# Optimization experiments

Measured on AMD Instinct MI355X. Metric: run time of the kernel, lower is better.

The kernel has to match this reference:

```python
import jax, jax.numpy as jnp
import numpy as np

D_MODEL = 1024
NUM_HEADS = 16
HEAD_DIM = D_MODEL // NUM_HEADS
NUM_KERNELS = 21


def tisa_bias(amp, off, sharp, seq_len):
    # amp/off/sharp: (H, K). Returns (H, L, L) translation-invariant bias.
    # Evaluate on the 2L-1 distinct relative distances, then gather (Toeplitz).
    d = jnp.arange(-(seq_len - 1), seq_len, dtype=amp.dtype)  # (2L-1,)
    # (H, K, 2L-1) -> sum over kernels -> (H, 2L-1)
    scores = jnp.sum(
        amp[:, :, None]
        * jnp.exp(-jnp.abs(sharp)[:, :, None] * (d[None, None, :] - off[:, :, None]) ** 2),
        axis=1,
    )
    i = jnp.arange(seq_len)
    rel_idx = i[None, :] - i[:, None] + (seq_len - 1)  # (L, L) in [0, 2L-2]
    return scores[:, rel_idx]  # (H, L, L)


def setup_inputs() -> dict:
    key = jax.random.key(0)
    ks = jax.random.split(key, 9)
    B, L = 4, 1024
    s = 0.02
    return {
        "x_q": jax.random.normal(ks[0], (B, L, D_MODEL), dtype=jnp.float32),
        "x_kv": jax.random.normal(ks[1], (B, L, D_MODEL), dtype=jnp.float32),
        "Wq": jax.random.normal(ks[2], (D_MODEL, D_MODEL), dtype=jnp.float32) * s,
        "Wm": jax.random.normal(ks[3], (D_MODEL, 2 * D_MODEL), dtype=jnp.float32) * s,
        "Wg": jax.random.normal(ks[4], (D_MODEL, 2 * D_MODEL), dtype=jnp.float32) * s,
        "bg": jnp.zeros((2 * D_MODEL,), dtype=jnp.float32),
        "tisa_amp": jax.random.normal(ks[5], (NUM_HEADS, NUM_KERNELS), dtype=jnp.float32) * 0.1,
        "tisa_off": jax.random.uniform(ks[6], (NUM_HEADS, NUM_KERNELS), dtype=jnp.float32, minval=-512.0, maxval=512.0),
        "tisa_sharp": jax.random.uniform(ks[7], (NUM_HEADS, NUM_KERNELS), dtype=jnp.float32, minval=1e-4, maxval=0.05),
    }


def reference(x_q, x_kv, Wq, Wm, Wg, bg, tisa_amp, tisa_off, tisa_sharp):
    B, Lq, _ = x_q.shape
    Lkv = x_kv.shape[1]
    H, Dh = NUM_HEADS, HEAD_DIM

    q = (x_q @ Wq).reshape(B, Lq, H, Dh).transpose(0, 2, 1, 3)        # (B,H,Lq,Dh)
    mem = (x_kv @ Wm)                                                 # (B,Lkv,2D)
    k = mem[..., :D_MODEL].reshape(B, Lkv, H, Dh).transpose(0, 2, 1, 3)
    v = mem[..., D_MODEL:].reshape(B, Lkv, H, Dh).transpose(0, 2, 1, 3)

    scale = 1.0 / jnp.sqrt(jnp.asarray(Dh, dtype=q.dtype))
    scores = jnp.einsum("bhqd,bhkd->bhqk", q, k) * scale              # (B,H,Lq,Lkv)
    scores = scores + tisa_bias(tisa_amp, tisa_off, tisa_sharp, Lkv)[None]
    weights = jax.nn.softmax(scores, axis=-1)

    attn = jnp.einsum("bhqk,bhkd->bhqd", weights, v)                  # (B,H,Lq,Dh)
    attn = attn.transpose(0, 2, 1, 3).reshape(B, Lq, D_MODEL)

    g = attn @ Wg + bg                                                # (B,Lq,2D)
    a, b = g[..., :D_MODEL], g[..., D_MODEL:]
    return a * jax.nn.sigmoid(b)
```

## Files before the change

### kernel.cpp

```cpp
#include <hip/hip_runtime.h>
#include <cstdint>
#include <cstddef>

typedef __attribute__((ext_vector_type(8))) short bf16x8;
typedef __attribute__((ext_vector_type(4))) float f32x4;

#define LOG2E 1.44269504f

__device__ __forceinline__ unsigned short f2bf(float x) {
  unsigned int u = __float_as_uint(x);
  u += 0x7FFFu + ((u >> 16) & 1u);
  return (unsigned short)(u >> 16);
}
__device__ __forceinline__ unsigned short f2bf_trunc(float x) {
  return (unsigned short)(__float_as_uint(x) >> 16);
}

__device__ __forceinline__ void gload_lds16(const void* g, void* l) {
  __builtin_amdgcn_global_load_lds(
      (const __attribute__((address_space(1))) unsigned int*)g,
      (__attribute__((address_space(3))) unsigned int*)l, 16, 0, 0);
}


__global__ void preproc(const float* __restrict__ x_q, const float* __restrict__ x_kv,
                        const float* __restrict__ Wq, const float* __restrict__ Wm,
                        const float* __restrict__ Wg,
                        const float* __restrict__ amp, const float* __restrict__ off,
                        const float* __restrict__ sharp,
                        ushort4* __restrict__ bXq, ushort4* __restrict__ bXkv,
                        unsigned short* __restrict__ dWq, unsigned short* __restrict__ dWm,
                        unsigned short* __restrict__ dWg, float* __restrict__ tab) {
  __shared__ float tile[32][33];
  const int blk = blockIdx.x;
  if (blk < 8192) {
    int i = blk * 256 + threadIdx.x;
    float4 v;
    ushort4* d;
    if (i < (1 << 20)) { v = ((const float4*)x_q)[i]; d = bXq + i; }
    else { int j = i - (1 << 20); v = ((const float4*)x_kv)[j]; d = bXkv + j; }
    ushort4 o;
    o.x = f2bf(v.x); o.y = f2bf(v.y); o.z = f2bf(v.z); o.w = f2bf(v.w);
    *d = o;
  } else if (blk < 14336) {
    int idx = blk - 8192;
    int z = idx >> 11, rem = idx & 2047;
    int bx = rem & 63, by = rem >> 6;
    const float* src = z == 0 ? Wq : (z == 1 ? Wm : Wg);
    unsigned short* dst = z == 0 ? dWq : (z == 1 ? dWm : dWg);
    int N = z == 0 ? 1024 : 2048;
    int nb = bx * 32, kb = by * 32;
    if (nb >= N) return;
    int tx = threadIdx.x & 31, ty = threadIdx.x >> 5;
#pragma unroll
    for (int r = ty; r < 32; r += 8)
      tile[r][tx] = src[(size_t)(kb + r) * N + nb + tx];
    __syncthreads();
#pragma unroll
    for (int r = ty; r < 32; r += 8)
      dst[(size_t)(nb + r) * 1024 + kb + tx] = f2bf(tile[tx][r]);
  } else {
    int h = blk - 14336;
    for (int idx = threadIdx.x; idx < 2047; idx += 256) {
      float d = (float)(idx - 1023);
      float acc = 0.f;
#pragma unroll
      for (int k = 0; k < 21; ++k) {
        float dd = d - off[h * 21 + k];
        acc += amp[h * 21 + k] * __expf(-fabsf(sharp[h * 21 + k]) * dd * dd);
      }
      tab[h * 2047 + idx] = acc * LOG2E;
    }
  }
}


__global__ __launch_bounds__(256, 4)
void qkv_gemm(const unsigned short* __restrict__ Xq,
              const unsigned short* __restrict__ Xkv,
              const unsigned short* __restrict__ WqT,
              const unsigned short* __restrict__ WmT,
              unsigned short* __restrict__ qbuf,
              unsigned short* __restrict__ kbuf,
              unsigned short* __restrict__ vtbuf) {
  __shared__ unsigned short sA[2][128 * 32];
  __shared__ unsigned short sB[2][128 * 32];
  const int bx = blockIdx.x;
  const bool isQ = bx < 8;
  const int ntile = (isQ ? bx : bx - 8) << 7;
  const unsigned short* A = isQ ? Xq : Xkv;
  const unsigned short* B = (isQ ? WqT : WmT) + (size_t)ntile * 1024;
  const int t = threadIdx.x, lane = t & 63, w = t >> 6;
  const int wm = (w >> 1) << 6, wn = (w & 1) << 6;
  const int mtile = blockIdx.y << 7;
  const int c = lane & 15, g = lane >> 4;
  const int srow = t >> 2, scol = (t & 3) << 3;
  const unsigned short* aP = A + (size_t)(mtile + srow) * 1024 + scol;
  const unsigned short* bP = B + (size_t)srow * 1024 + scol;
  const int lo = srow * 32 + scol;

  gload_lds16(aP, &sA[0][lo]);
  gload_lds16(aP + 64 * 1024, &sA[0][lo + 64 * 32]);
  gload_lds16(bP, &sB[0][lo]);
  gload_lds16(bP + 64 * 1024, &sB[0][lo + 64 * 32]);
  __syncthreads();

  f32x4 acc[4][4] = {};
  for (int kt = 0; kt < 32; ++kt) {
    const int cur = kt & 1;
    if (kt + 1 < 32) {
      const int ko = (kt + 1) * 32;
      gload_lds16(aP + ko, &sA[1 - cur][lo]);
      gload_lds16(aP + 64 * 1024 + ko, &sA[1 - cur][lo + 64 * 32]);
      gload_lds16(bP + ko, &sB[1 - cur][lo]);
      gload_lds16(bP + 64 * 1024 + ko, &sB[1 - cur][lo + 64 * 32]);
    }
    bf16x8 af[4], bfr[4];
#pragma unroll
    for (int i = 0; i < 4; ++i) {
      af[i]  = *(const bf16x8*)&sA[cur][(wm + i * 16 + c) * 32 + g * 8];
      bfr[i] = *(const bf16x8*)&sB[cur][(wn + i * 16 + c) * 32 + g * 8];
    }
#pragma unroll
    for (int i = 0; i < 4; ++i)
#pragma unroll
      for (int j = 0; j < 4; ++j)
        acc[i][j] = __builtin_amdgcn_mfma_f32_16x16x32_bf16(af[i], bfr[j], acc[i][j], 0, 0, 0);
    __syncthreads();
  }

  const int row0 = mtile + wm + (g << 2);
  const int col0 = ntile + wn + c;
  if (isQ) {
#pragma unroll
    for (int i = 0; i < 4; ++i)
#pragma unroll
      for (int j = 0; j < 4; ++j) {
        int r = row0 + i * 16, cl = col0 + j * 16;
#pragma unroll
        for (int ri = 0; ri < 4; ++ri)
          qbuf[(size_t)(r + ri) * 1024 + cl] = f2bf(acc[i][j][ri] * (0.125f * LOG2E));
      }
  } else {
#pragma unroll
    for (int i = 0; i < 4; ++i)
#pragma unroll
      for (int j = 0; j < 4; ++j) {
        int r = row0 + i * 16, cl = col0 + j * 16;
        if (cl < 1024) {
#pragma unroll
          for (int ri = 0; ri < 4; ++ri)
            kbuf[(size_t)(r + ri) * 1024 + cl] = f2bf(acc[i][j][ri]);
        } else {
          int d = cl - 1024;
          int hh = d >> 6, dh = d & 63;
          int bb = r >> 10, ll = r & 1023;
          ushort4 pk;
          pk.x = f2bf(acc[i][j][0]);
          pk.y = f2bf(acc[i][j][1]);
          pk.z = f2bf(acc[i][j][2]);
          pk.w = f2bf(acc[i][j][3]);
          *(ushort4*)&vtbuf[((size_t)((bb * 16 + hh) * 64 + dh) << 10) + ll] = pk;
        }
      }
  }
}


__global__ __launch_bounds__(512)
void attn_kernel(const unsigned short* __restrict__ qbuf,
                 const unsigned short* __restrict__ kbuf,
                 const unsigned short* __restrict__ vtbuf,
                 const float* __restrict__ biasTab,
                 unsigned short* __restrict__ attnb) {
  const int h = blockIdx.x & 15, b = blockIdx.x >> 4, qt = blockIdx.y;
  __shared__ unsigned short sK[2][64 * 64];
  __shared__ unsigned short sV[3][64 * 64];
  __shared__ unsigned short sP[2][128 * 64];
  __shared__ float sLsum[2][128];
  const int t = threadIdx.x, lane = t & 63, w = t >> 6;
  const int c = lane & 15, g = lane >> 4;
  const int rg = w >> 1, cg = w & 1;

  const int r = t >> 3, ch = (t & 7) ^ (r & 7);

  const unsigned short* qsrc = qbuf + (size_t)(b * 1024 + qt * 128) * 1024 + h * 64;
  const unsigned short* ksrc = kbuf + (size_t)(b * 1024) * 1024 + h * 64;
  const unsigned short* vsrc = vtbuf + (size_t)((b * 16 + h) * 64) * 1024;

  unsigned short* sQ = &sP[0][0];
  gload_lds16(qsrc + (size_t)r * 1024 + ch * 8, &sQ[t * 8]);
  gload_lds16(qsrc + (size_t)(r + 64) * 1024 + ch * 8, &sQ[4096 + t * 8]);
  gload_lds16(ksrc + (size_t)r * 1024 + ch * 8, &sK[0][t * 8]);
  gload_lds16(vsrc + (size_t)r * 1024 + ch * 8, &sV[0][t * 8]);
  __syncthreads();

  bf16x8 aq[2][2];
#pragma unroll
  for (int rf = 0; rf < 2; ++rf) {
    int row = rg * 32 + rf * 16 + c;
#pragma unroll
    for (int ks = 0; ks < 2; ++ks)
      aq[rf][ks] = *(const bf16x8*)&sQ[row * 64 + (((ks * 4 + g) ^ (row & 7)) * 8)];
  }
  __syncthreads();

  f32x4 o[2][2] = {};
  float lsum[2][4] = {};
  const float* bb = biasTab + h * 2047 + 1023 + cg * 32 + c - qt * 128 - rg * 32 - g * 4;

  int vcur = 0, vnx = 1;
  for (int kv = 0; kv < 16; ++kv) {
    const int cur = kv & 1;

    const float* bk = bb + kv * 64;
    f32x4 s[2][2];
#pragma unroll
    for (int rf = 0; rf < 2; ++rf)
#pragma unroll
      for (int nf = 0; nf < 2; ++nf)
#pragma unroll
        for (int ri = 0; ri < 4; ++ri)
          s[rf][nf][ri] = bk[(nf - rf) * 16 - ri];

    if (kv + 1 < 16) {
      gload_lds16(ksrc + (size_t)((kv + 1) * 64 + r) * 1024 + ch * 8, &sK[1 - cur][t * 8]);
      gload_lds16(vsrc + (size_t)r * 1024 + (kv + 1) * 64 + ch * 8, &sV[vnx][t * 8]);
    }

#pragma unroll
    for (int nf = 0; nf < 2; ++nf) {
      int krow = cg * 32 + nf * 16 + c;
      bf16x8 k0 = *(const bf16x8*)&sK[cur][krow * 64 + (((g) ^ (krow & 7)) * 8)];
      bf16x8 k1 = *(const bf16x8*)&sK[cur][krow * 64 + (((4 + g) ^ (krow & 7)) * 8)];
#pragma unroll
      for (int rf = 0; rf < 2; ++rf) {
        s[rf][nf] = __builtin_amdgcn_mfma_f32_16x16x32_bf16(aq[rf][0], k0, s[rf][nf], 0, 0, 0);
        s[rf][nf] = __builtin_amdgcn_mfma_f32_16x16x32_bf16(aq[rf][1], k1, s[rf][nf], 0, 0, 0);
      }
    }

#pragma unroll
    for (int rf = 0; rf < 2; ++rf)
#pragma unroll
      for (int nf = 0; nf < 2; ++nf)
#pragma unroll
        for (int ri = 0; ri < 4; ++ri) {
          float e = exp2f(s[rf][nf][ri]);
          lsum[rf][ri] += e;
          int prow = rg * 32 + rf * 16 + g * 4 + ri;
          int chunk = cg * 4 + nf * 2 + (c >> 3);
          sP[cur][prow * 64 + ((chunk ^ (prow & 7)) * 8) + (c & 7)] = f2bf_trunc(e);
        }
    __syncthreads();

    bf16x8 ap[2][2];
#pragma unroll
    for (int rf = 0; rf < 2; ++rf) {
      int row = rg * 32 + rf * 16 + c;
#pragma unroll
      for (int ks = 0; ks < 2; ++ks)
        ap[rf][ks] = *(const bf16x8*)&sP[cur][row * 64 + (((ks * 4 + g) ^ (row & 7)) * 8)];
    }
#pragma unroll
    for (int df = 0; df < 2; ++df) {
      int vrow = cg * 32 + df * 16 + c;
      bf16x8 v0 = *(const bf16x8*)&sV[vcur][vrow * 64 + (((g) ^ (vrow & 7)) * 8)];
      bf16x8 v1 = *(const bf16x8*)&sV[vcur][vrow * 64 + (((4 + g) ^ (vrow & 7)) * 8)];
#pragma unroll
      for (int rf = 0; rf < 2; ++rf) {
        o[rf][df] = __builtin_amdgcn_mfma_f32_16x16x32_bf16(ap[rf][0], v0, o[rf][df], 0, 0, 0);
        o[rf][df] = __builtin_amdgcn_mfma_f32_16x16x32_bf16(ap[rf][1], v1, o[rf][df], 0, 0, 0);
      }
    }
    vcur = vnx;
    vnx = (vnx == 2) ? 0 : vnx + 1;
  }

#pragma unroll
  for (int off = 1; off < 16; off <<= 1)
#pragma unroll
    for (int rf = 0; rf < 2; ++rf)
#pragma unroll
      for (int ri = 0; ri < 4; ++ri)
        lsum[rf][ri] += __shfl_xor(lsum[rf][ri], off, 64);
  if (c == 0) {
#pragma unroll
    for (int rf = 0; rf < 2; ++rf)
#pragma unroll
      for (int ri = 0; ri < 4; ++ri)
        sLsum[cg][rg * 32 + rf * 16 + g * 4 + ri] = lsum[rf][ri];
  }
  __syncthreads();

  unsigned short* obase = attnb +
      (size_t)(b * 1024 + qt * 128 + rg * 32 + g * 4) * 1024 + h * 64 + cg * 32 + c;
#pragma unroll
  for (int rf = 0; rf < 2; ++rf)
#pragma unroll
    for (int ri = 0; ri < 4; ++ri) {
      int row = rg * 32 + rf * 16 + g * 4 + ri;
      float rinv = 1.0f / (sLsum[0][row] + sLsum[1][row]);
#pragma unroll
      for (int df = 0; df < 2; ++df)
        obase[(size_t)(rf * 16 + ri) * 1024 + df * 16] = f2bf(o[rf][df][ri] * rinv);
    }
}


__global__ __launch_bounds__(256, 4)
void out_gemm(const unsigned short* __restrict__ A,
              const unsigned short* __restrict__ WgT,
              const float* __restrict__ bg,
              float* __restrict__ out) {
  __shared__ unsigned short sA[2][64 * 32];
  __shared__ unsigned short sB[2][128 * 32];
  const int nb = blockIdx.x;
  const int mtile = blockIdx.y << 6;
  const int t = threadIdx.x, lane = t & 63, w = t >> 6;
  const int c = lane & 15, g = lane >> 4;
  const int rm = w >> 1, cn = w & 1;
  const int srow = t >> 2, scol = (t & 3) << 3;
  const unsigned short* aP = A + (size_t)(mtile + srow) * 1024 + scol;
  const unsigned short* bP0 = WgT + (size_t)(nb * 64 + srow) * 1024 + scol;
  const unsigned short* bP1 = WgT + (size_t)(1024 + nb * 64 + srow) * 1024 + scol;
  const int lo = srow * 32 + scol;

  gload_lds16(aP, &sA[0][lo]);
  gload_lds16(bP0, &sB[0][lo]);
  gload_lds16(bP1, &sB[0][lo + 64 * 32]);
  __syncthreads();

  f32x4 acc[2][4] = {};
  for (int kt = 0; kt < 32; ++kt) {
    const int cur = kt & 1;
    if (kt + 1 < 32) {
      const int ko = (kt + 1) * 32;
      gload_lds16(aP + ko, &sA[1 - cur][lo]);
      gload_lds16(bP0 + ko, &sB[1 - cur][lo]);
      gload_lds16(bP1 + ko, &sB[1 - cur][lo + 64 * 32]);
    }
    bf16x8 af[2], bfr[4];
#pragma unroll
    for (int i = 0; i < 2; ++i)
      af[i] = *(const bf16x8*)&sA[cur][(rm * 32 + i * 16 + c) * 32 + g * 8];
#pragma unroll
    for (int jj = 0; jj < 2; ++jj) {
      bfr[jj]     = *(const bf16x8*)&sB[cur][(cn * 32 + jj * 16 + c) * 32 + g * 8];
      bfr[jj + 2] = *(const bf16x8*)&sB[cur][(64 + cn * 32 + jj * 16 + c) * 32 + g * 8];
    }
#pragma unroll
    for (int i = 0; i < 2; ++i)
#pragma unroll
      for (int j = 0; j < 4; ++j)
        acc[i][j] = __builtin_amdgcn_mfma_f32_16x16x32_bf16(af[i], bfr[j], acc[i][j], 0, 0, 0);
    __syncthreads();
  }

#pragma unroll
  for (int i = 0; i < 2; ++i) {
    int row0 = mtile + rm * 32 + i * 16 + (g << 2);
#pragma unroll
    for (int jj = 0; jj < 2; ++jj) {
      int col = nb * 64 + cn * 32 + jj * 16 + c;
      float ba = bg[col];
      float bbv = bg[1024 + col];
#pragma unroll
      for (int ri = 0; ri < 4; ++ri) {
        float av = acc[i][jj][ri] + ba;
        float bv = acc[i][jj + 2][ri] + bbv;
        out[(size_t)(row0 + ri) * 1024 + col] = av / (1.f + exp2f(-LOG2E * bv));
      }
    }
  }
}


extern "C" void kernel_launch(void* const* d_in, const int* in_sizes, int n_in,
                              void* d_out, int out_size, void* d_ws, size_t ws_size,
                              hipStream_t stream) {
  const float* x_q   = (const float*)d_in[0];
  const float* x_kv  = (const float*)d_in[1];
  const float* Wq    = (const float*)d_in[2];
  const float* Wm    = (const float*)d_in[3];
  const float* Wg    = (const float*)d_in[4];
  const float* bg    = (const float*)d_in[5];
  const float* amp   = (const float*)d_in[6];
  const float* off   = (const float*)d_in[7];
  const float* sharp = (const float*)d_in[8];
  float* out = (float*)d_out;

  char* ws = (char*)d_ws;
  size_t o = 0;
  auto alloc = [&](size_t bytes) {
    char* p = ws + o;
    o += (bytes + 255) & ~(size_t)255;
    return p;
  };
  unsigned short* bXq   = (unsigned short*)alloc(4096ull * 1024 * 2);
  unsigned short* bXkv  = (unsigned short*)alloc(4096ull * 1024 * 2);
  unsigned short* bWqT  = (unsigned short*)alloc(1024ull * 1024 * 2);
  unsigned short* bWmT  = (unsigned short*)alloc(2048ull * 1024 * 2);
  unsigned short* bWgT  = (unsigned short*)alloc(2048ull * 1024 * 2);
  float*          biasT = (float*)alloc(16ull * 2047 * 4);
  unsigned short* qbuf  = (unsigned short*)alloc(4096ull * 1024 * 2);
  unsigned short* kbuf  = (unsigned short*)alloc(4096ull * 1024 * 2);
  unsigned short* vtbuf = (unsigned short*)alloc(4096ull * 1024 * 2);
  unsigned short* attnb = (unsigned short*)alloc(4096ull * 1024 * 2);
  if (ws_size < o) return;

  preproc<<<14352, 256, 0, stream>>>(x_q, x_kv, Wq, Wm, Wg, amp, off, sharp,
                                     (ushort4*)bXq, (ushort4*)bXkv,
                                     bWqT, bWmT, bWgT, biasT);
  qkv_gemm<<<dim3(24, 32), 256, 0, stream>>>(bXq, bXkv, bWqT, bWmT, qbuf, kbuf, vtbuf);
  attn_kernel<<<dim3(64, 8), 512, 0, stream>>>(qbuf, kbuf, vtbuf, biasT, attnb);
  out_gemm<<<dim3(16, 64), 256, 0, stream>>>(attnb, bWgT, bg, out);
}
```

Measured before the change: 209.0 us.

## Use 2-wave blocks with 64x128 per-wave tiles in projection GEMMs

Both the QKV and output GEMMs move from 4 waves per block to 2, with each wave computing a 64x128 tile (32 MFMA accumulators). The output GEMM also grows from a 64-row to a 128-row tile, so the grid halves, and B rows are loaded interleaved so each wave's gate and value columns line up. The aim is more MFMA work per LDS fragment load and fewer blocks, in exchange for higher register pressure, lower occupancy and fewer waves to hide latency.

```diff
diff --git a/kernel.cpp b/kernel.cpp
--- a/kernel.cpp
+++ b/kernel.cpp
@@ -75,7 +75,7 @@
 }
 
 
-__global__ __launch_bounds__(256, 4)
+__global__ __launch_bounds__(128, 2)
 void qkv_gemm(const unsigned short* __restrict__ Xq,
               const unsigned short* __restrict__ Xkv,
               const unsigned short* __restrict__ WqT,
@@ -91,52 +91,53 @@
   const unsigned short* A = isQ ? Xq : Xkv;
   const unsigned short* B = (isQ ? WqT : WmT) + (size_t)ntile * 1024;
   const int t = threadIdx.x, lane = t & 63, w = t >> 6;
-  const int wm = (w >> 1) << 6, wn = (w & 1) << 6;
   const int mtile = blockIdx.y << 7;
   const int c = lane & 15, g = lane >> 4;
-  const int srow = t >> 2, scol = (t & 3) << 3;
-  const unsigned short* aP = A + (size_t)(mtile + srow) * 1024 + scol;
-  const unsigned short* bP = B + (size_t)srow * 1024 + scol;
-  const int lo = srow * 32 + scol;
-
-  gload_lds16(aP, &sA[0][lo]);
-  gload_lds16(aP + 64 * 1024, &sA[0][lo + 64 * 32]);
-  gload_lds16(bP, &sB[0][lo]);
-  gload_lds16(bP + 64 * 1024, &sB[0][lo + 64 * 32]);
+  const int rr = lane >> 2, cc = (lane & 3) << 3;
+  const unsigned short* aBase = A + (size_t)(mtile + w * 64 + rr) * 1024 + cc;
+  const unsigned short* bBase = B + (size_t)(w * 64 + rr) * 1024 + cc;
+  const int lo = (w * 64 + rr) * 32 + cc;
+
+#pragma unroll
+  for (int j = 0; j < 4; ++j) {
+    gload_lds16(aBase + (size_t)j * 16 * 1024, &sA[0][lo + j * 512]);
+    gload_lds16(bBase + (size_t)j * 16 * 1024, &sB[0][lo + j * 512]);
+  }
   __syncthreads();
 
-  f32x4 acc[4][4] = {};
+  f32x4 acc[4][8] = {};
   for (int kt = 0; kt < 32; ++kt) {
     const int cur = kt & 1;
     if (kt + 1 < 32) {
       const int ko = (kt + 1) * 32;
-      gload_lds16(aP + ko, &sA[1 - cur][lo]);
-      gload_lds16(aP + 64 * 1024 + ko, &sA[1 - cur][lo + 64 * 32]);
-      gload_lds16(bP + ko, &sB[1 - cur][lo]);
-      gload_lds16(bP + 64 * 1024 + ko, &sB[1 - cur][lo + 64 * 32]);
-    }
-    bf16x8 af[4], bfr[4];
-#pragma unroll
-    for (int i = 0; i < 4; ++i) {
-      af[i]  = *(const bf16x8*)&sA[cur][(wm + i * 16 + c) * 32 + g * 8];
-      bfr[i] = *(const bf16x8*)&sB[cur][(wn + i * 16 + c) * 32 + g * 8];
-    }
-#pragma unroll
-    for (int i = 0; i < 4; ++i)
-#pragma unroll
-      for (int j = 0; j < 4; ++j)
+#pragma unroll
+      for (int j = 0; j < 4; ++j) {
+        gload_lds16(aBase + (size_t)j * 16 * 1024 + ko, &sA[1 - cur][lo + j * 512]);
+        gload_lds16(bBase + (size_t)j * 16 * 1024 + ko, &sB[1 - cur][lo + j * 512]);
+      }
+    }
+    bf16x8 af[4], bfr[8];
+#pragma unroll
+    for (int i = 0; i < 4; ++i)
+      af[i] = *(const bf16x8*)&sA[cur][(w * 64 + i * 16 + c) * 32 + g * 8];
+#pragma unroll
+    for (int j = 0; j < 8; ++j)
+      bfr[j] = *(const bf16x8*)&sB[cur][(j * 16 + c) * 32 + g * 8];
+#pragma unroll
+    for (int i = 0; i < 4; ++i)
+#pragma unroll
+      for (int j = 0; j < 8; ++j)
         acc[i][j] = __builtin_amdgcn_mfma_f32_16x16x32_bf16(af[i], bfr[j], acc[i][j], 0, 0, 0);
     __syncthreads();
   }
 
-  const int row0 = mtile + wm + (g << 2);
-  const int col0 = ntile + wn + c;
+  const int row0 = mtile + w * 64 + (g << 2);
   if (isQ) {
 #pragma unroll
     for (int i = 0; i < 4; ++i)
 #pragma unroll
-      for (int j = 0; j < 4; ++j) {
-        int r = row0 + i * 16, cl = col0 + j * 16;
+      for (int j = 0; j < 8; ++j) {
+        int r = row0 + i * 16, cl = ntile + j * 16 + c;
 #pragma unroll
         for (int ri = 0; ri < 4; ++ri)
           qbuf[(size_t)(r + ri) * 1024 + cl] = f2bf(acc[i][j][ri] * (0.125f * LOG2E));
@@ -145,8 +146,8 @@
 #pragma unroll
     for (int i = 0; i < 4; ++i)
 #pragma unroll
-      for (int j = 0; j < 4; ++j) {
-        int r = row0 + i * 16, cl = col0 + j * 16;
+      for (int j = 0; j < 8; ++j) {
+        int r = row0 + i * 16, cl = ntile + j * 16 + c;
         if (cl < 1024) {
 #pragma unroll
           for (int ri = 0; ri < 4; ++ri)
@@ -308,68 +309,76 @@
 }
 
 
-__global__ __launch_bounds__(256, 4)
+__global__ __launch_bounds__(128, 2)
 void out_gemm(const unsigned short* __restrict__ A,
               const unsigned short* __restrict__ WgT,
               const float* __restrict__ bg,
               float* __restrict__ out) {
-  __shared__ unsigned short sA[2][64 * 32];
+  __shared__ unsigned short sA[2][128 * 32];
   __shared__ unsigned short sB[2][128 * 32];
   const int nb = blockIdx.x;
-  const int mtile = blockIdx.y << 6;
+  const int mtile = blockIdx.y << 7;
   const int t = threadIdx.x, lane = t & 63, w = t >> 6;
   const int c = lane & 15, g = lane >> 4;
-  const int rm = w >> 1, cn = w & 1;
-  const int srow = t >> 2, scol = (t & 3) << 3;
-  const unsigned short* aP = A + (size_t)(mtile + srow) * 1024 + scol;
-  const unsigned short* bP0 = WgT + (size_t)(nb * 64 + srow) * 1024 + scol;
-  const unsigned short* bP1 = WgT + (size_t)(1024 + nb * 64 + srow) * 1024 + scol;
-  const int lo = srow * 32 + scol;
-
-  gload_lds16(aP, &sA[0][lo]);
-  gload_lds16(bP0, &sB[0][lo]);
-  gload_lds16(bP1, &sB[0][lo + 64 * 32]);
+  const int rr = lane >> 2, cc = (lane & 3) << 3;
+  const unsigned short* aBase = A + (size_t)(mtile + w * 64 + rr) * 1024 + cc;
+  const unsigned short* bBase[4];
+#pragma unroll
+  for (int j = 0; j < 4; ++j) {
+    int p = w * 64 + j * 16;
+    int q = p >> 5;
+    int grow = ((q & 1) ? 1024 : 0) + nb * 64 + (q >> 1) * 32 + (p & 31) + rr;
+    bBase[j] = WgT + (size_t)grow * 1024 + cc;
+  }
+  const int lo = (w * 64 + rr) * 32 + cc;
+
+#pragma unroll
+  for (int j = 0; j < 4; ++j) {
+    gload_lds16(aBase + (size_t)j * 16 * 1024, &sA[0][lo + j * 512]);
+    gload_lds16(bBase[j], &sB[0][lo + j * 512]);
+  }
   __syncthreads();
 
-  f32x4 acc[2][4] = {};
+  f32x4 acc[4][8] = {};
   for (int kt = 0; kt < 32; ++kt) {
     const int cur = kt & 1;
     if (kt + 1 < 32) {
       const int ko = (kt + 1) * 32;
-      gload_lds16(aP + ko, &sA[1 - cur][lo]);
-      gload_lds16(bP0 + ko, &sB[1 - cur][lo]);
-      gload_lds16(bP1 + ko, &sB[1 - cur][lo + 64 * 32]);
-    }
-    bf16x8 af[2], bfr[4];
-#pragma unroll
-    for (int i = 0; i < 2; ++i)
-      af[i] = *(const bf16x8*)&sA[cur][(rm * 32 + i * 16 + c) * 32 + g * 8];
-#pragma unroll
-    for (int jj = 0; jj < 2; ++jj) {
-      bfr[jj]     = *(const bf16x8*)&sB[cur][(cn * 32 + jj * 16 + c) * 32 + g * 8];
-      bfr[jj + 2] = *(const bf16x8*)&sB[cur][(64 + cn * 32 + jj * 16 + c) * 32 + g * 8];
-    }
-#pragma unroll
-    for (int i = 0; i < 2; ++i)
-#pragma unroll
-      for (int j = 0; j < 4; ++j)
+#pragma unroll
+      for (int j = 0; j < 4; ++j) {
+        gload_lds16(aBase + (size_t)j * 16 * 1024 + ko, &sA[1 - cur][lo + j * 512]);
+        gload_lds16(bBase[j] + ko, &sB[1 - cur][lo + j * 512]);
+      }
+    }
+    bf16x8 af[4], bfr[8];
+#pragma unroll
+    for (int i = 0; i < 4; ++i)
+      af[i] = *(const bf16x8*)&sA[cur][(w * 64 + i * 16 + c) * 32 + g * 8];
+#pragma unroll
+    for (int j = 0; j < 8; ++j)
+      bfr[j] = *(const bf16x8*)&sB[cur][(j * 16 + c) * 32 + g * 8];
+#pragma unroll
+    for (int i = 0; i < 4; ++i)
+#pragma unroll
+      for (int j = 0; j < 8; ++j)
         acc[i][j] = __builtin_amdgcn_mfma_f32_16x16x32_bf16(af[i], bfr[j], acc[i][j], 0, 0, 0);
     __syncthreads();
   }
 
-#pragma unroll
-  for (int i = 0; i < 2; ++i) {
-    int row0 = mtile + rm * 32 + i * 16 + (g << 2);
-#pragma unroll
-    for (int jj = 0; jj < 2; ++jj) {
-      int col = nb * 64 + cn * 32 + jj * 16 + c;
+  const int row0 = mtile + w * 64 + (g << 2);
+#pragma unroll
+  for (int i = 0; i < 4; ++i) {
+#pragma unroll
+    for (int jj = 0; jj < 4; ++jj) {
+      int ja = (jj & 1) + (jj >> 1) * 4;
+      int col = nb * 64 + (jj >> 1) * 32 + (jj & 1) * 16 + c;
       float ba = bg[col];
       float bbv = bg[1024 + col];
 #pragma unroll
       for (int ri = 0; ri < 4; ++ri) {
-        float av = acc[i][jj][ri] + ba;
-        float bv = acc[i][jj + 2][ri] + bbv;
-        out[(size_t)(row0 + ri) * 1024 + col] = av / (1.f + exp2f(-LOG2E * bv));
+        float av = acc[i][ja][ri] + ba;
+        float bv = acc[i][ja + 2][ri] + bbv;
+        out[(size_t)(row0 + i * 16 + ri) * 1024 + col] = av / (1.f + exp2f(-LOG2E * bv));
       }
     }
   }
@@ -412,7 +421,7 @@
   preproc<<<14352, 256, 0, stream>>>(x_q, x_kv, Wq, Wm, Wg, amp, off, sharp,
                                      (ushort4*)bXq, (ushort4*)bXkv,
                                      bWqT, bWmT, bWgT, biasT);
-  qkv_gemm<<<dim3(24, 32), 256, 0, stream>>>(bXq, bXkv, bWqT, bWmT, qbuf, kbuf, vtbuf);
+  qkv_gemm<<<dim3(24, 32), 128, 0, stream>>>(bXq, bXkv, bWqT, bWmT, qbuf, kbuf, vtbuf);
   attn_kernel<<<dim3(64, 8), 512, 0, stream>>>(qbuf, kbuf, vtbuf, biasT, attnb);
-  out_gemm<<<dim3(16, 64), 256, 0, stream>>>(attnb, bWgT, bg, out);
-}
+  out_gemm<<<dim3(16, 32), 128, 0, stream>>>(attnb, bWgT, bg, out);
+}
```

After: 232.1 us. 1.11x slower.
